# Kernel optimization log

Hardware: AMD Instinct MI355X
Metric: run time of the kernel (lower is better)

## Reference

```python
import jax, jax.numpy as jnp
import numpy as np

N_REC = 3
TEMP = 1.0
BAL_W = 0.01
Z_W = 0.001


def setup_inputs() -> dict:
    key = jax.random.key(0)
    kx, kw = jax.random.split(key)
    x = jax.random.normal(kx, (4, 4096, 2048), dtype=jnp.float32)
    W = 0.02 * jax.random.normal(kw, (N_REC, 2048), dtype=jnp.float32)  # nn.Linear(d_model, n_rec, bias=False), std=0.02
    return {"x": x, "W": W, "recursion_idx": 0}


def _compact(mask, cur_gate, max_k):
    """Vectorized version of the per-batch nonzero/pad loop.
    mask: [B,T] bool, cur_gate: [B,T] float. Returns sel [B,max_k], gv [B,max_k]."""
    counts = jnp.sum(mask, axis=-1)  # [B]
    # stable argsort pushes active (key=0) positions to the front, in order
    key = jnp.where(mask, 0, 1).astype(jnp.int32)
    order = jnp.argsort(key, axis=-1, stable=True)  # [B,T]
    # position j clamps to last valid index (replicates pad-with-last behavior)
    pos = jnp.minimum(jnp.arange(max_k)[None, :], jnp.maximum(counts - 1, 0)[:, None])
    sel = jnp.take_along_axis(order, pos, axis=1)  # [B,max_k]
    empty = (counts == 0)[:, None]
    sel = jnp.where(empty, 0, sel)
    gv = jnp.take_along_axis(cur_gate, sel, axis=1)
    gv = jnp.where(empty, jnp.float32(0.0), gv)
    return sel, gv


def reference(x, W, recursion_idx):
    # router linear + softmax + argmax (one-shot token-choice assignment)
    logits = jnp.einsum('btd,nd->btn', x / TEMP, W)  # [B,T,N_REC]
    gates = jax.nn.softmax(logits, axis=-1)
    assign = jnp.argmax(gates, axis=-1)  # [B,T]
    active_mask = assign >= recursion_idx
    cur_gate = gates[:, :, min(recursion_idx, N_REC - 1)]  # [B,T]
    # max_k is data-dependent (eager, outside jit)
    max_k = max(1, int(jnp.max(jnp.sum(active_mask, axis=-1))))
    sel, gv = _compact(active_mask, cur_gate, max_k)
    selected = sel[..., None]          # [B,max_k,1] int
    gate_weights = gv[..., None]       # [B,max_k,1]
    # training-mode losses (recursion_idx == 0 path)
    fracs = jnp.mean(jax.nn.one_hot(assign, N_REC, dtype=jnp.float32), axis=(0, 1))
    aux_loss = BAL_W * jnp.sum((fracs - 1.0 / N_REC) ** 2)
    z = jax.scipy.special.logsumexp(logits, axis=-1)
    z_loss = Z_W * jnp.mean(z ** 2)
    return selected, gate_weights, logits[:, :, :1], aux_loss, z_loss
```

## Files before the change

kernel.cpp:

```cpp
#include <hip/hip_runtime.h>
#include <hip/hip_bf16.h>

#define B_    4
#define T_    4096
#define D_    2048
#define NTOK  (B_ * T_)
#define NREC  3
#define BAL_W 0.01f
#define Z_W   0.001f
#define ABLK  1024
#define ATHR  512

typedef __attribute__((ext_vector_type(4))) float float4v;

__global__ __launch_bounds__(ATHR) void tcr7_phaseA(
    const float* __restrict__ x,
    const float* __restrict__ w,
    const int* __restrict__ ridx_p,
    float* __restrict__ out_f,
    float4v* __restrict__ partials)
{
    __shared__ float s_w[NREC * D_];
    {
        const float4v* src = reinterpret_cast<const float4v*>(w);
        float4v*       dst = reinterpret_cast<float4v*>(s_w);
#pragma unroll
        for (int i = 0; i < (NREC * D_ / 4) / ATHR; ++i)
            dst[i * ATHR + threadIdx.x] = src[i * ATHR + threadIdx.x];
    }
    __syncthreads();

    const int ridx = ridx_p[0];
    const int jc   = ridx < (NREC - 1) ? (ridx < 0 ? 0 : ridx) : (NREC - 1);
    const int lane = threadIdx.x & 63;
    const int wv   = threadIdx.x >> 6;
    const int wid  = (blockIdx.x * ATHR + threadIdx.x) >> 6;
    const int nw   = (gridDim.x * ATHR) >> 6;

    float z2 = 0.f, c0 = 0.f, c1 = 0.f, c2 = 0.f;

    for (int t = wid; t < NTOK; t += nw) {
        const float* xp = x + (size_t)t * D_;
        float4v xv[8];
#pragma unroll
        for (int j = 0; j < 8; ++j)
            xv[j] = *reinterpret_cast<const float4v*>(xp + (j * 64 + lane) * 4);

        float a0 = 0.f, a1 = 0.f, a2 = 0.f;
#pragma unroll
        for (int j = 0; j < 8; ++j) {
            const int kb = (j * 64 + lane) * 4;
            const float4v w0 = *reinterpret_cast<const float4v*>(&s_w[kb]);
            const float4v w1 = *reinterpret_cast<const float4v*>(&s_w[D_ + kb]);
            const float4v w2 = *reinterpret_cast<const float4v*>(&s_w[2 * D_ + kb]);
#pragma unroll
            for (int e = 0; e < 4; ++e) {
                a0 = fmaf(xv[j][e], w0[e], a0);
                a1 = fmaf(xv[j][e], w1[e], a1);
                a2 = fmaf(xv[j][e], w2[e], a2);
            }
        }
#pragma unroll
        for (int off = 32; off > 0; off >>= 1) {
            a0 += __shfl_xor(a0, off);
            a1 += __shfl_xor(a1, off);
            a2 += __shfl_xor(a2, off);
        }
        if (lane == 0) {
            const float m  = fmaxf(a0, fmaxf(a1, a2));
            const float e0 = expf(a0 - m), e1 = expf(a1 - m), e2 = expf(a2 - m);
            const float s  = e0 + e1 + e2;
            const float z  = m + logf(s);
            int   assign = 0; float best = a0;
            if (a1 > best) { best = a1; assign = 1; }
            if (a2 > best) { best = a2; assign = 2; }
            const float g = (jc == 0 ? e0 : (jc == 1 ? e1 : e2)) / s;

            out_f[NTOK + t]     = (assign >= ridx) ? g : -g;
            out_f[2 * NTOK + t] = a0;

            z2 += z * z;
            if (assign == 0) c0 += 1.f; else if (assign == 1) c1 += 1.f; else c2 += 1.f;
        }
    }

    __shared__ float4v s_part[ATHR / 64];
    if (lane == 0) {
        float4v p; p[0] = z2; p[1] = c0; p[2] = c1; p[3] = c2;
        s_part[wv] = p;
    }
    __syncthreads();
    if (threadIdx.x == 0) {
        float4v p = s_part[0];
#pragma unroll
        for (int i = 1; i < ATHR / 64; ++i) {
            const float4v q = s_part[i];
#pragma unroll
            for (int e = 0; e < 4; ++e) p[e] += q[e];
        }
        partials[blockIdx.x] = p;
    }
}

__global__ __launch_bounds__(1024) void tcr7_phaseB(
    const float4v* __restrict__ partials,
    float* __restrict__ out_f)
{
    __shared__ int      s_ws[16];
    __shared__ unsigned s_sel[T_];
    __shared__ float    s_g[T_];
    __shared__ float4v  s_red[16];
    const int b    = blockIdx.x;
    const int tid  = threadIdx.x;
    const int lane = tid & 63;
    const int wv   = tid >> 6;
    const int base = b * T_;

    float g[4]; int f[4]; int loc = 0;
#pragma unroll
    for (int r = 0; r < 4; ++r) {
        g[r] = out_f[NTOK + base + tid * 4 + r];
        f[r] = (g[r] > 0.f) ? 1 : 0;
        loc += f[r];
    }
    int isc = loc;
#pragma unroll
    for (int off = 1; off < 64; off <<= 1) {
        const int u = __shfl_up(isc, off);
        if (lane >= off) isc += u;
    }
    if (lane == 63) s_ws[wv] = isc;
    __syncthreads();
    int wbase = 0, cnt = 0;
#pragma unroll
    for (int i = 0; i < 16; ++i) {
        const int v = s_ws[i];
        cnt += v;
        if (i < wv) wbase += v;
    }
    int pos = wbase + isc - loc;
#pragma unroll
    for (int r = 0; r < 4; ++r) {
        if (f[r] && (unsigned)pos < (unsigned)T_) {
            s_sel[pos] = (unsigned)(tid * 4 + r);
            s_g[pos]   = g[r];
            ++pos;
        }
    }
    __syncthreads();

#pragma unroll
    for (int r = 0; r < 4; ++r) {
        const int k = tid + r * 1024;
        float selv, gv;
        if (cnt == 0) { selv = 0.f; gv = 0.f; }
        else {
            const int kk = (k < cnt) ? k : (cnt - 1);
            selv = (float)s_sel[kk];
            gv   = s_g[kk];
        }
        out_f[base + k]        = selv;
        out_f[NTOK + base + k] = gv;
    }

    float4v p;
    if (b == 0) p = partials[tid];
    else { p[0] = 0.f; p[1] = 0.f; p[2] = 0.f; p[3] = 0.f; }
#pragma unroll
    for (int off = 32; off > 0; off >>= 1) {
#pragma unroll
        for (int e = 0; e < 4; ++e) p[e] += __shfl_xor(p[e], off);
    }
    if (lane == 0) s_red[wv] = p;
    __syncthreads();
    if (b == 0 && tid == 0) {
        float4v q = s_red[0];
#pragma unroll
        for (int i = 1; i < 16; ++i) {
            const float4v r2 = s_red[i];
#pragma unroll
            for (int e = 0; e < 4; ++e) q[e] += r2[e];
        }
        const float inv = 1.0f / (float)NTOK;
        float aux = 0.f;
#pragma unroll
        for (int n = 0; n < NREC; ++n) {
            const float d = q[1 + n] * inv - (1.0f / 3.0f);
            aux = fmaf(d, d, aux);
        }
        out_f[3 * NTOK + 0] = BAL_W * aux;
        out_f[3 * NTOK + 1] = Z_W * q[0] * inv;
    }
}

extern "C" void kernel_launch(void* const* d_in, const int* in_sizes, int n_in,
                              void* d_out, int out_size, void* d_ws, size_t ws_size,
                              hipStream_t stream) {
    const float* x  = (const float*)d_in[0];
    const float* w  = (const float*)d_in[1];
    const int* ridx = (const int*)d_in[2];
    float* out_f = (float*)d_out;
    float4v* partials = (float4v*)d_ws;

    tcr7_phaseA<<<dim3(ABLK), dim3(ATHR), 0, stream>>>(x, w, ridx, out_f, partials);
    tcr7_phaseB<<<dim3(B_), dim3(1024), 0, stream>>>(partials, out_f);
}
```

Before: 33.63 us.

## Process two tokens per wavefront with no loop, using a larger grid of smaller blocks

Each wavefront now loads two token rows at once and reuses every shared-memory weight load for both dot products. The grid-stride loop is removed, so the grid of 2048 blocks of 256 threads covers all tokens exactly once. The aim is to put more memory loads in flight per wave and to halve LDS weight traffic per token. In exchange it uses more registers, repeats the shared-weight staging in twice as many blocks, and phase B now sums 2048 partials.

```diff
diff --git a/kernel.cpp b/kernel.cpp
--- a/kernel.cpp
+++ b/kernel.cpp
@@ -8,12 +8,12 @@
 #define NREC  3
 #define BAL_W 0.01f
 #define Z_W   0.001f
-#define ABLK  1024
-#define ATHR  512
+#define ABLK  2048
+#define ATHR  256
 
 typedef __attribute__((ext_vector_type(4))) float float4v;
 
-__global__ __launch_bounds__(ATHR) void tcr7_phaseA(
+__global__ __launch_bounds__(ATHR) void tcr8_phaseA(
     const float* __restrict__ x,
     const float* __restrict__ w,
     const int* __restrict__ ridx_p,
@@ -35,65 +35,76 @@
     const int lane = threadIdx.x & 63;
     const int wv   = threadIdx.x >> 6;
     const int wid  = (blockIdx.x * ATHR + threadIdx.x) >> 6;
-    const int nw   = (gridDim.x * ATHR) >> 6;
-
-    float z2 = 0.f, c0 = 0.f, c1 = 0.f, c2 = 0.f;
-
-    for (int t = wid; t < NTOK; t += nw) {
-        const float* xp = x + (size_t)t * D_;
-        float4v xv[8];
-#pragma unroll
-        for (int j = 0; j < 8; ++j)
-            xv[j] = *reinterpret_cast<const float4v*>(xp + (j * 64 + lane) * 4);
-
-        float a0 = 0.f, a1 = 0.f, a2 = 0.f;
-#pragma unroll
-        for (int j = 0; j < 8; ++j) {
-            const int kb = (j * 64 + lane) * 4;
-            const float4v w0 = *reinterpret_cast<const float4v*>(&s_w[kb]);
-            const float4v w1 = *reinterpret_cast<const float4v*>(&s_w[D_ + kb]);
-            const float4v w2 = *reinterpret_cast<const float4v*>(&s_w[2 * D_ + kb]);
-#pragma unroll
-            for (int e = 0; e < 4; ++e) {
-                a0 = fmaf(xv[j][e], w0[e], a0);
-                a1 = fmaf(xv[j][e], w1[e], a1);
-                a2 = fmaf(xv[j][e], w2[e], a2);
-            }
-        }
-#pragma unroll
-        for (int off = 32; off > 0; off >>= 1) {
-            a0 += __shfl_xor(a0, off);
-            a1 += __shfl_xor(a1, off);
-            a2 += __shfl_xor(a2, off);
-        }
-        if (lane == 0) {
-            const float m  = fmaxf(a0, fmaxf(a1, a2));
-            const float e0 = expf(a0 - m), e1 = expf(a1 - m), e2 = expf(a2 - m);
-            const float s  = e0 + e1 + e2;
-            const float z  = m + logf(s);
-            int   assign = 0; float best = a0;
-            if (a1 > best) { best = a1; assign = 1; }
-            if (a2 > best) { best = a2; assign = 2; }
-            const float g = (jc == 0 ? e0 : (jc == 1 ? e1 : e2)) / s;
-
-            out_f[NTOK + t]     = (assign >= ridx) ? g : -g;
-            out_f[2 * NTOK + t] = a0;
-
-            z2 += z * z;
-            if (assign == 0) c0 += 1.f; else if (assign == 1) c1 += 1.f; else c2 += 1.f;
-        }
-    }
-
-    __shared__ float4v s_part[ATHR / 64];
-    if (lane == 0) {
-        float4v p; p[0] = z2; p[1] = c0; p[2] = c1; p[3] = c2;
-        s_part[wv] = p;
+    const int t0   = wid * 2;
+
+    const float* xp0 = x + (size_t)t0 * D_;
+    float4v xv0[8], xv1[8];
+#pragma unroll
+    for (int j = 0; j < 8; ++j) {
+        xv0[j] = *reinterpret_cast<const float4v*>(xp0 + (j * 64 + lane) * 4);
+        xv1[j] = *reinterpret_cast<const float4v*>(xp0 + D_ + (j * 64 + lane) * 4);
+    }
+
+    float a0 = 0.f, a1 = 0.f, a2 = 0.f;
+    float b0 = 0.f, b1 = 0.f, b2 = 0.f;
+#pragma unroll
+    for (int j = 0; j < 8; ++j) {
+        const int kb = (j * 64 + lane) * 4;
+        const float4v w0 = *reinterpret_cast<const float4v*>(&s_w[kb]);
+        const float4v w1 = *reinterpret_cast<const float4v*>(&s_w[D_ + kb]);
+        const float4v w2 = *reinterpret_cast<const float4v*>(&s_w[2 * D_ + kb]);
+#pragma unroll
+        for (int e = 0; e < 4; ++e) {
+            a0 = fmaf(xv0[j][e], w0[e], a0);
+            a1 = fmaf(xv0[j][e], w1[e], a1);
+            a2 = fmaf(xv0[j][e], w2[e], a2);
+            b0 = fmaf(xv1[j][e], w0[e], b0);
+            b1 = fmaf(xv1[j][e], w1[e], b1);
+            b2 = fmaf(xv1[j][e], w2[e], b2);
+        }
+    }
+#pragma unroll
+    for (int off = 32; off > 0; off >>= 1) {
+        a0 += __shfl_xor(a0, off);
+        a1 += __shfl_xor(a1, off);
+        a2 += __shfl_xor(a2, off);
+        b0 += __shfl_xor(b0, off);
+        b1 += __shfl_xor(b1, off);
+        b2 += __shfl_xor(b2, off);
+    }
+
+    __shared__ float4v s_part[(ATHR / 64) * 2];
+    if ((lane & 31) == 0) {
+        const int hi = lane >> 5;
+        const int t  = t0 + hi;
+        const float l0 = hi ? b0 : a0;
+        const float l1 = hi ? b1 : a1;
+        const float l2 = hi ? b2 : a2;
+
+        const float m  = fmaxf(l0, fmaxf(l1, l2));
+        const float e0 = expf(l0 - m), e1 = expf(l1 - m), e2 = expf(l2 - m);
+        const float s  = e0 + e1 + e2;
+        const float z  = m + logf(s);
+        int   assign = 0; float best = l0;
+        if (l1 > best) { best = l1; assign = 1; }
+        if (l2 > best) { best = l2; assign = 2; }
+        const float g = (jc == 0 ? e0 : (jc == 1 ? e1 : e2)) / s;
+
+        out_f[NTOK + t]     = (assign >= ridx) ? g : -g;
+        out_f[2 * NTOK + t] = l0;
+
+        float4v p;
+        p[0] = z * z;
+        p[1] = (assign == 0) ? 1.f : 0.f;
+        p[2] = (assign == 1) ? 1.f : 0.f;
+        p[3] = (assign == 2) ? 1.f : 0.f;
+        s_part[wv * 2 + hi] = p;
     }
     __syncthreads();
     if (threadIdx.x == 0) {
         float4v p = s_part[0];
 #pragma unroll
-        for (int i = 1; i < ATHR / 64; ++i) {
+        for (int i = 1; i < (ATHR / 64) * 2; ++i) {
             const float4v q = s_part[i];
 #pragma unroll
             for (int e = 0; e < 4; ++e) p[e] += q[e];
@@ -102,7 +113,7 @@
     }
 }
 
-__global__ __launch_bounds__(1024) void tcr7_phaseB(
+__global__ __launch_bounds__(1024) void tcr8_phaseB(
     const float4v* __restrict__ partials,
     float* __restrict__ out_f)
 {
@@ -164,8 +175,12 @@
     }
 
     float4v p;
-    if (b == 0) p = partials[tid];
-    else { p[0] = 0.f; p[1] = 0.f; p[2] = 0.f; p[3] = 0.f; }
+    if (b == 0) {
+        const float4v pa = partials[tid];
+        const float4v pb = partials[tid + 1024];
+#pragma unroll
+        for (int e = 0; e < 4; ++e) p[e] = pa[e] + pb[e];
+    } else { p[0] = 0.f; p[1] = 0.f; p[2] = 0.f; p[3] = 0.f; }
 #pragma unroll
     for (int off = 32; off > 0; off >>= 1) {
 #pragma unroll
@@ -202,6 +217,6 @@
     float* out_f = (float*)d_out;
     float4v* partials = (float4v*)d_ws;
 
-    tcr7_phaseA<<<dim3(ABLK), dim3(ATHR), 0, stream>>>(x, w, ridx, out_f, partials);
-    tcr7_phaseB<<<dim3(B_), dim3(1024), 0, stream>>>(partials, out_f);
+    tcr8_phaseA<<<dim3(ABLK), dim3(ATHR), 0, stream>>>(x, w, ridx, out_f, partials);
+    tcr8_phaseB<<<dim3(B_), dim3(1024), 0, stream>>>(partials, out_f);
 }
```

Measured after the change: 32.57 us. 1.03x faster.

## Double-buffer token loads with fixed four tokens per wave and nontemporal loads

Applied to the files above, without the earlier changes.

Replaces the grid-stride token loop with a fixed assignment of four consecutive tokens per wavefront. Two register buffers are ping-ponged so the next token's row is loaded while the current one is being reduced. The block size drops to 256 threads with a min-blocks launch bound, and x and W are read with nontemporal loads to avoid polluting the cache. Fewer waves are resident, so memory-level parallelism now relies on the explicit prefetch, and register pressure rises from holding two token buffers.

```diff
diff --git a/kernel.cpp b/kernel.cpp
--- a/kernel.cpp
+++ b/kernel.cpp
@@ -9,11 +9,19 @@
 #define BAL_W 0.01f
 #define Z_W   0.001f
 #define ABLK  1024
-#define ATHR  512
+#define ATHR  256
 
 typedef __attribute__((ext_vector_type(4))) float float4v;
 
-__global__ __launch_bounds__(ATHR) void tcr7_phaseA(
+__device__ __forceinline__ void load_tok(const float* __restrict__ xp, int lane,
+                                         float4v v[8]) {
+#pragma unroll
+    for (int j = 0; j < 8; ++j)
+        v[j] = __builtin_nontemporal_load(
+            reinterpret_cast<const float4v*>(xp + (j * 64 + lane) * 4));
+}
+
+__global__ __launch_bounds__(ATHR, 4) void tcr10_phaseA(
     const float* __restrict__ x,
     const float* __restrict__ w,
     const int* __restrict__ ridx_p,
@@ -26,7 +34,8 @@
         float4v*       dst = reinterpret_cast<float4v*>(s_w);
 #pragma unroll
         for (int i = 0; i < (NREC * D_ / 4) / ATHR; ++i)
-            dst[i * ATHR + threadIdx.x] = src[i * ATHR + threadIdx.x];
+            dst[i * ATHR + threadIdx.x] =
+                __builtin_nontemporal_load(src + i * ATHR + threadIdx.x);
     }
     __syncthreads();
 
@@ -35,17 +44,11 @@
     const int lane = threadIdx.x & 63;
     const int wv   = threadIdx.x >> 6;
     const int wid  = (blockIdx.x * ATHR + threadIdx.x) >> 6;
-    const int nw   = (gridDim.x * ATHR) >> 6;
+    const int t0   = wid * 4;
 
     float z2 = 0.f, c0 = 0.f, c1 = 0.f, c2 = 0.f;
 
-    for (int t = wid; t < NTOK; t += nw) {
-        const float* xp = x + (size_t)t * D_;
-        float4v xv[8];
-#pragma unroll
-        for (int j = 0; j < 8; ++j)
-            xv[j] = *reinterpret_cast<const float4v*>(xp + (j * 64 + lane) * 4);
-
+    auto process = [&](const float4v v[8], int t) {
         float a0 = 0.f, a1 = 0.f, a2 = 0.f;
 #pragma unroll
         for (int j = 0; j < 8; ++j) {
@@ -55,9 +58,9 @@
             const float4v w2 = *reinterpret_cast<const float4v*>(&s_w[2 * D_ + kb]);
 #pragma unroll
             for (int e = 0; e < 4; ++e) {
-                a0 = fmaf(xv[j][e], w0[e], a0);
-                a1 = fmaf(xv[j][e], w1[e], a1);
-                a2 = fmaf(xv[j][e], w2[e], a2);
+                a0 = fmaf(v[j][e], w0[e], a0);
+                a1 = fmaf(v[j][e], w1[e], a1);
+                a2 = fmaf(v[j][e], w2[e], a2);
             }
         }
 #pragma unroll
@@ -82,7 +85,18 @@
             z2 += z * z;
             if (assign == 0) c0 += 1.f; else if (assign == 1) c1 += 1.f; else c2 += 1.f;
         }
-    }
+    };
+
+    const float* xp = x + (size_t)t0 * D_;
+    float4v bufA[8], bufB[8];
+    load_tok(xp, lane, bufA);
+    load_tok(xp + D_, lane, bufB);
+    process(bufA, t0);
+    load_tok(xp + 2 * (size_t)D_, lane, bufA);
+    process(bufB, t0 + 1);
+    load_tok(xp + 3 * (size_t)D_, lane, bufB);
+    process(bufA, t0 + 2);
+    process(bufB, t0 + 3);
 
     __shared__ float4v s_part[ATHR / 64];
     if (lane == 0) {
@@ -102,7 +116,7 @@
     }
 }
 
-__global__ __launch_bounds__(1024) void tcr7_phaseB(
+__global__ __launch_bounds__(1024) void tcr10_phaseB(
     const float4v* __restrict__ partials,
     float* __restrict__ out_f)
 {
@@ -202,6 +216,6 @@
     float* out_f = (float*)d_out;
     float4v* partials = (float4v*)d_ws;
 
-    tcr7_phaseA<<<dim3(ABLK), dim3(ATHR), 0, stream>>>(x, w, ridx, out_f, partials);
-    tcr7_phaseB<<<dim3(B_), dim3(1024), 0, stream>>>(partials, out_f);
-}
+    tcr10_phaseA<<<dim3(ABLK), dim3(ATHR), 0, stream>>>(x, w, ridx, out_f, partials);
+    tcr10_phaseB<<<dim3(B_), dim3(1024), 0, stream>>>(partials, out_f);
+}
```

Measured after the change: 42.74 us. 1.27x slower.

## Split each token's dot product across slices with LDS reduction and nontemporal loads

Applied to the files above, without the earlier changes.

Phase A no longer gives each token to one wave. Each 256-thread block now handles 16 tokens, with 16 threads per token each reducing a contiguous 128-element slice. Partial dot products are combined through shared memory instead of wave shuffles. Loads of x are double-buffered in registers and use nontemporal hints. This aims to raise memory-level parallelism and drop the per-token shuffle reductions, but each load instruction now scatters lanes across rows, which may hurt coalescing on a bandwidth-bound kernel.

```diff
diff --git a/kernel.cpp b/kernel.cpp
--- a/kernel.cpp
+++ b/kernel.cpp
@@ -8,12 +8,14 @@
 #define NREC  3
 #define BAL_W 0.01f
 #define Z_W   0.001f
-#define ABLK  1024
-#define ATHR  512
+#define TPB   16
+#define SLC   16
+#define ABLK  (NTOK / TPB)
+#define ATHR  (TPB * SLC)
 
 typedef __attribute__((ext_vector_type(4))) float float4v;
 
-__global__ __launch_bounds__(ATHR) void tcr7_phaseA(
+__global__ __launch_bounds__(ATHR) void tcr12_phaseA(
     const float* __restrict__ x,
     const float* __restrict__ w,
     const int* __restrict__ ridx_p,
@@ -26,83 +28,105 @@
         float4v*       dst = reinterpret_cast<float4v*>(s_w);
 #pragma unroll
         for (int i = 0; i < (NREC * D_ / 4) / ATHR; ++i)
-            dst[i * ATHR + threadIdx.x] = src[i * ATHR + threadIdx.x];
-    }
-    __syncthreads();
-
-    const int ridx = ridx_p[0];
-    const int jc   = ridx < (NREC - 1) ? (ridx < 0 ? 0 : ridx) : (NREC - 1);
-    const int lane = threadIdx.x & 63;
-    const int wv   = threadIdx.x >> 6;
-    const int wid  = (blockIdx.x * ATHR + threadIdx.x) >> 6;
-    const int nw   = (gridDim.x * ATHR) >> 6;
-
-    float z2 = 0.f, c0 = 0.f, c1 = 0.f, c2 = 0.f;
-
-    for (int t = wid; t < NTOK; t += nw) {
-        const float* xp = x + (size_t)t * D_;
-        float4v xv[8];
-#pragma unroll
-        for (int j = 0; j < 8; ++j)
-            xv[j] = *reinterpret_cast<const float4v*>(xp + (j * 64 + lane) * 4);
-
-        float a0 = 0.f, a1 = 0.f, a2 = 0.f;
-#pragma unroll
-        for (int j = 0; j < 8; ++j) {
-            const int kb = (j * 64 + lane) * 4;
-            const float4v w0 = *reinterpret_cast<const float4v*>(&s_w[kb]);
-            const float4v w1 = *reinterpret_cast<const float4v*>(&s_w[D_ + kb]);
-            const float4v w2 = *reinterpret_cast<const float4v*>(&s_w[2 * D_ + kb]);
+            dst[i * ATHR + threadIdx.x] =
+                __builtin_nontemporal_load(src + i * ATHR + threadIdx.x);
+    }
+    __syncthreads();
+
+    const int tid = threadIdx.x;
+    const int ti  = tid & (TPB - 1);
+    const int s   = tid >> 4;
+    const int t   = blockIdx.x * TPB + ti;
+
+    const float4v* xv =
+        reinterpret_cast<const float4v*>(x + (size_t)t * D_ + s * (D_ / SLC));
+    const float* wbase = s_w + s * (D_ / SLC);
+
+    float a0 = 0.f, a1 = 0.f, a2 = 0.f;
+
+    float4v A[8], Bv[8];
+#pragma unroll
+    for (int u = 0; u < 8; ++u) A[u]  = __builtin_nontemporal_load(xv + u);
+#pragma unroll
+    for (int u = 0; u < 8; ++u) Bv[u] = __builtin_nontemporal_load(xv + 8 + u);
+
+    auto proc = [&](const float4v (&buf)[8], int jb) {
+#pragma unroll
+        for (int u = 0; u < 8; ++u) {
+            const int off = (jb + u) * 4;
+            const float4v w0 = *reinterpret_cast<const float4v*>(wbase + off);
+            const float4v w1 = *reinterpret_cast<const float4v*>(wbase + D_ + off);
+            const float4v w2 = *reinterpret_cast<const float4v*>(wbase + 2 * D_ + off);
 #pragma unroll
             for (int e = 0; e < 4; ++e) {
-                a0 = fmaf(xv[j][e], w0[e], a0);
-                a1 = fmaf(xv[j][e], w1[e], a1);
-                a2 = fmaf(xv[j][e], w2[e], a2);
+                a0 = fmaf(buf[u][e], w0[e], a0);
+                a1 = fmaf(buf[u][e], w1[e], a1);
+                a2 = fmaf(buf[u][e], w2[e], a2);
             }
         }
-#pragma unroll
-        for (int off = 32; off > 0; off >>= 1) {
-            a0 += __shfl_xor(a0, off);
-            a1 += __shfl_xor(a1, off);
-            a2 += __shfl_xor(a2, off);
-        }
-        if (lane == 0) {
-            const float m  = fmaxf(a0, fmaxf(a1, a2));
-            const float e0 = expf(a0 - m), e1 = expf(a1 - m), e2 = expf(a2 - m);
-            const float s  = e0 + e1 + e2;
-            const float z  = m + logf(s);
-            int   assign = 0; float best = a0;
-            if (a1 > best) { best = a1; assign = 1; }
-            if (a2 > best) { best = a2; assign = 2; }
-            const float g = (jc == 0 ? e0 : (jc == 1 ? e1 : e2)) / s;
-
-            out_f[NTOK + t]     = (assign >= ridx) ? g : -g;
-            out_f[2 * NTOK + t] = a0;
-
-            z2 += z * z;
-            if (assign == 0) c0 += 1.f; else if (assign == 1) c1 += 1.f; else c2 += 1.f;
-        }
-    }
-
-    __shared__ float4v s_part[ATHR / 64];
-    if (lane == 0) {
-        float4v p; p[0] = z2; p[1] = c0; p[2] = c1; p[3] = c2;
-        s_part[wv] = p;
-    }
-    __syncthreads();
-    if (threadIdx.x == 0) {
-        float4v p = s_part[0];
-#pragma unroll
-        for (int i = 1; i < ATHR / 64; ++i) {
-            const float4v q = s_part[i];
-#pragma unroll
-            for (int e = 0; e < 4; ++e) p[e] += q[e];
-        }
-        partials[blockIdx.x] = p;
+    };
+
+    proc(A, 0);
+#pragma unroll
+    for (int u = 0; u < 8; ++u) A[u] = __builtin_nontemporal_load(xv + 16 + u);
+    proc(Bv, 8);
+#pragma unroll
+    for (int u = 0; u < 8; ++u) Bv[u] = __builtin_nontemporal_load(xv + 24 + u);
+    proc(A, 16);
+    proc(Bv, 24);
+
+    __shared__ float   s_dots[TPB][SLC + 1][3];
+    __shared__ float4v s_p[TPB];
+    s_dots[ti][s][0] = a0;
+    s_dots[ti][s][1] = a1;
+    s_dots[ti][s][2] = a2;
+    __syncthreads();
+
+    if (tid < TPB) {
+        float d0 = 0.f, d1 = 0.f, d2 = 0.f;
+#pragma unroll
+        for (int q = 0; q < SLC; ++q) {
+            d0 += s_dots[tid][q][0];
+            d1 += s_dots[tid][q][1];
+            d2 += s_dots[tid][q][2];
+        }
+        const int ridx = ridx_p[0];
+        const int jc   = ridx < (NREC - 1) ? (ridx < 0 ? 0 : ridx) : (NREC - 1);
+        const int t2   = blockIdx.x * TPB + tid;
+
+        const float m  = fmaxf(d0, fmaxf(d1, d2));
+        const float e0 = expf(d0 - m), e1 = expf(d1 - m), e2 = expf(d2 - m);
+        const float sm = e0 + e1 + e2;
+        const float z  = m + logf(sm);
+        int   assign = 0; float best = d0;
+        if (d1 > best) { best = d1; assign = 1; }
+        if (d2 > best) { best = d2; assign = 2; }
+        const float g = (jc == 0 ? e0 : (jc == 1 ? e1 : e2)) / sm;
+
+        out_f[NTOK + t2]     = (assign >= ridx) ? g : -g;
+        out_f[2 * NTOK + t2] = d0;
+
+        float4v p;
+        p[0] = z * z;
+        p[1] = (assign == 0) ? 1.f : 0.f;
+        p[2] = (assign == 1) ? 1.f : 0.f;
+        p[3] = (assign == 2) ? 1.f : 0.f;
+        s_p[tid] = p;
+    }
+    __syncthreads();
+    if (tid == 0) {
+        float4v q = s_p[0];
+#pragma unroll
+        for (int i = 1; i < TPB; ++i) {
+            const float4v r2 = s_p[i];
+#pragma unroll
+            for (int e = 0; e < 4; ++e) q[e] += r2[e];
+        }
+        partials[blockIdx.x] = q;
     }
 }
 
-__global__ __launch_bounds__(1024) void tcr7_phaseB(
+__global__ __launch_bounds__(1024) void tcr12_phaseB(
     const float4v* __restrict__ partials,
     float* __restrict__ out_f)
 {
@@ -202,6 +226,6 @@
     float* out_f = (float*)d_out;
     float4v* partials = (float4v*)d_ws;
 
-    tcr7_phaseA<<<dim3(ABLK), dim3(ATHR), 0, stream>>>(x, w, ridx, out_f, partials);
-    tcr7_phaseB<<<dim3(B_), dim3(1024), 0, stream>>>(partials, out_f);
+    tcr12_phaseA<<<dim3(ABLK), dim3(ATHR), 0, stream>>>(x, w, ridx, out_f, partials);
+    tcr12_phaseB<<<dim3(B_),   dim3(1024), 0, stream>>>(partials, out_f);
 }
```

Result: slower. 72.47 us (+115.5%).
